# Performance work log

Hardware: AMD Instinct MI355X
Metric: run time of the kernel (lower is better)

Reference implementation:

```python
import jax, jax.numpy as jnp
import numpy as np

FM = 80            # feature_maps
N_ROUNDS = 32
NORM_EPS = 1e-3
LOSS_EPS = 1e-8


def _relu6(x):
    return jnp.clip(x, 0.0, 6.0)


def _norm(x):
    # tf.nn.moments over axis 0 + batch_normalization (no scale/offset)
    mean = jnp.mean(x, axis=0, keepdims=True)
    var = jnp.var(x, axis=0, keepdims=True)
    return (x - mean) * jax.lax.rsqrt(var + NORM_EPS)


def setup_inputs() -> dict:
    key = jax.random.key(0)
    n_vars, n_clauses, n_graphs, lits_per_clause = 100000, 420000, 100, 3
    n_cells = n_clauses * lits_per_clause
    ks = jax.random.split(key, 24)

    lit_var = jax.random.randint(ks[0], (n_cells,), 0, n_vars, dtype=jnp.int32)
    lit_neg = jax.random.randint(ks[1], (n_cells,), 0, 2, dtype=jnp.int32)
    clause_idx = jnp.repeat(jnp.arange(n_clauses, dtype=jnp.int32), lits_per_clause)
    clause_graph = jnp.repeat(jnp.arange(n_graphs, dtype=jnp.int32), n_clauses // n_graphs)

    def dense(k, fi, fo):
        return jax.random.normal(k, (fi, fo), jnp.float32) / np.sqrt(fi)

    inp = dict(
        lit_var=lit_var, lit_neg=lit_neg, clause_idx=clause_idx, clause_graph=clause_graph,
        n_vars=n_vars, n_clauses=n_clauses, n_graphs=n_graphs,
        L_init_scale=jnp.float32(1.0 / np.sqrt(FM)),
        C_init_scale=jnp.float32(1.0 / np.sqrt(FM)),
        LC_scale=jnp.float32(0.1), CL_scale=jnp.float32(0.1),
        # L_update MLP: in=3*FM (L, CL_msgs, flip(L)) -> hidden 3*FM relu6 -> FM
        Lu_W0=dense(ks[2], 3 * FM, 3 * FM), Lu_b0=jnp.zeros((3 * FM,), jnp.float32),
        Lu_W1=dense(ks[3], 3 * FM, FM),     Lu_b1=jnp.zeros((FM,), jnp.float32),
        # C_update MLP: in=2*FM (C, LC_msgs) -> hidden 2*FM relu6 -> FM
        Cu_W0=dense(ks[4], 2 * FM, 2 * FM), Cu_b0=jnp.zeros((2 * FM,), jnp.float32),
        Cu_W1=dense(ks[5], 2 * FM, FM),     Cu_b1=jnp.zeros((FM,), jnp.float32),
        # V_score MLP: in=2*FM -> 3 hidden relu6 layers of 2*FM -> 1
        Vs_W0=dense(ks[6], 2 * FM, 2 * FM), Vs_b0=jnp.zeros((2 * FM,), jnp.float32),
        Vs_W1=dense(ks[7], 2 * FM, 2 * FM), Vs_b1=jnp.zeros((2 * FM,), jnp.float32),
        Vs_W2=dense(ks[8], 2 * FM, 2 * FM), Vs_b2=jnp.zeros((2 * FM,), jnp.float32),
        Vs_W3=dense(ks[9], 2 * FM, 1),      Vs_b3=jnp.zeros((1,), jnp.float32),
    )
    return inp


def reference(lit_var, lit_neg, clause_idx, clause_graph, n_vars, n_clauses, n_graphs,
              L_init_scale, C_init_scale, LC_scale, CL_scale,
              Lu_W0, Lu_b0, Lu_W1, Lu_b1,
              Cu_W0, Cu_b0, Cu_W1, Cu_b1,
              Vs_W0, Vs_b0, Vs_W1, Vs_b1, Vs_W2, Vs_b2, Vs_W3, Vs_b3):
    n_lits = 2 * n_vars
    lit_row = lit_var + lit_neg * n_vars          # row in L for each cell
    sign = (1 - 2 * lit_neg).astype(jnp.float32)  # +1 positive literal, -1 negated

    def mlp_L(x):
        return _relu6(x @ Lu_W0 + Lu_b0) @ Lu_W1 + Lu_b1

    def mlp_C(x):
        return _relu6(x @ Cu_W0 + Cu_b0) @ Cu_W1 + Cu_b1

    def v_score(x):
        h = _relu6(x @ Vs_W0 + Vs_b0)
        h = _relu6(h @ Vs_W1 + Vs_b1)
        h = _relu6(h @ Vs_W2 + Vs_b2)
        return h @ Vs_W3 + Vs_b3

    def flip(L):
        return jnp.concatenate([L[n_vars:], L[:n_vars]], axis=0)

    def per_round_loss(logits):
        # softplus_mixed_loss over ragged clauses of signed literals
        lit_vals = logits[lit_var, 0] * sign                         # [n_cells]
        clause_sum = jax.ops.segment_sum(jax.nn.softplus(lit_vals), clause_idx,
                                         num_segments=n_clauses)     # [n_clauses]
        vc = jnp.exp(-clause_sum)
        per_clause = vc * (-jnp.log(1.0 - vc + LOSS_EPS))
        per_graph = jax.ops.segment_sum(per_clause, clause_graph, num_segments=n_graphs)
        return jnp.sum(jnp.sqrt(per_graph + 1e-6))

    L0 = jnp.ones((n_lits, FM), jnp.float32) * L_init_scale
    C0 = jnp.ones((n_clauses, FM), jnp.float32) * C_init_scale

    def round_fn(carry, _):
        L, C, loss = carry
        # CL^T @ L  (sparse gather + segment-sum over clause cells)
        LC_msgs = jax.ops.segment_sum(L[lit_row], clause_idx, num_segments=n_clauses) * LC_scale
        C = _norm(mlp_C(jnp.concatenate([C, LC_msgs], axis=-1)))
        # adj @ C  (scatter-add clause features back to literal rows)
        CL_msgs = jax.ops.segment_sum(C[clause_idx], lit_row, num_segments=n_lits) * CL_scale
        L = _norm(mlp_L(jnp.concatenate([L, CL_msgs, flip(L)], axis=-1)))
        V = jnp.concatenate([L[:n_vars], L[n_vars:]], axis=1)        # [n_vars, 2*FM]
        logits = v_score(V)
        loss = loss + per_round_loss(logits)
        return (L, C, loss), None

    (L, C, loss), _ = jax.lax.scan(round_fn, (L0, C0, jnp.float32(0.0)), None, length=N_ROUNDS)
    # final-round logits (recomputed from the final L state, identical math)
    logits = v_score(jnp.concatenate([L[:n_vars], L[n_vars:]], axis=1))
    return logits, loss / N_ROUNDS
```

## Files before the change

### kernel.cpp

```cpp
#include <hip/hip_runtime.h>
#include <hip/hip_fp8.h>
#include <math.h>


#define NROUNDS 32
#define NORM_EPS 1e-3f
#define LOSS_EPS 1e-8f

static constexpr int NV_CONST = 100000;
static constexpr int NG_CONST = 100;

typedef __attribute__((ext_vector_type(8))) short short8;
typedef __attribute__((ext_vector_type(8))) unsigned char uchar8;
typedef __attribute__((ext_vector_type(16))) unsigned char uchar16;
typedef __attribute__((ext_vector_type(4))) float f32x4;

__device__ __forceinline__ short f2bf(float f) {
    union { float f; unsigned u; } x; x.f = f;
    unsigned r = x.u + 0x7fffu + ((x.u >> 16) & 1u);
    return (short)(r >> 16);
}
__device__ __forceinline__ float bf2f(short s) {
    union { unsigned u; float f; } x; x.u = ((unsigned)(unsigned short)s) << 16;
    return x.f;
}
__device__ __forceinline__ unsigned char f2q8(float f) {
    f = fminf(fmaxf(f, -448.f), 448.f);
    __hip_fp8_e4m3 t(f);
    return t.__x;
}
__device__ __forceinline__ float q82f(unsigned char b) {
    __hip_fp8_e4m3 t; t.__x = b;
    return (float)t;
}

__device__ __forceinline__ int xcd_swz(int b, int nb) {
    int q = nb >> 3, r = nb & 7;
    int xcd = b & 7, idx = b >> 3;
    return (xcd < r ? xcd * (q + 1) : r * (q + 1) + (xcd - r) * q) + idx;
}


__global__ void k_zero_i(int* __restrict__ p, int n) {
    int i = blockIdx.x * 256 + threadIdx.x;
    if (i < n) p[i] = 0;
}
__global__ void k_fill_b(short* __restrict__ p, int n, const float* __restrict__ vp) {
    int i = blockIdx.x * 256 + threadIdx.x;
    if (i < n) p[i] = f2bf(*vp);
}
__global__ void k_fill_q8(unsigned char* __restrict__ p, int n, const float* __restrict__ vp) {
    int i = blockIdx.x * 256 + threadIdx.x;
    if (i < n) p[i] = f2q8(*vp);
}
__global__ void k_copy_int(int* __restrict__ dst, const int* __restrict__ src, int n) {
    int i = blockIdx.x * 256 + threadIdx.x;
    if (i < n) dst[i] = src[i];
}
__global__ void k_init_slabs(float* __restrict__ slabC, float* __restrict__ slabL,
                             float* __restrict__ loss_a, float nclf, float nlf) {
    int i = blockIdx.x * 256 + threadIdx.x;
    if (i < 33 * 160) {
        slabC[i] = (i >= 80 && i < 160) ? nclf * (1.f - NORM_EPS) : 0.f;
        slabL[i] = (i >= 80 && i < 160) ? nlf * (1.f - NORM_EPS) : 0.f;
    }
    if (i == 0) loss_a[0] = 0.f;
}

__global__ void k_litrow(const int* __restrict__ lit_var, const int* __restrict__ lit_neg,
                         int* __restrict__ litrow, int* __restrict__ cellpk,
                         int* __restrict__ counts, int* __restrict__ fhist,
                         int ncell, int nv) {
    int i = blockIdx.x * 256 + threadIdx.x;
    if (i < ncell) {
        int vv = lit_var[i], ng = lit_neg[i];
        int r = vv + ng * nv;
        litrow[i] = r;
        cellpk[i] = vv | (ng << 31);
        atomicAdd(&counts[r], 1);
        if (i % 3 == 0) atomicAdd(&fhist[r], 1);
    }
}

__launch_bounds__(1024)
__global__ void k_scan4(const int* __restrict__ counts, int* __restrict__ row_ptr,
                        int n, int total) {
    __shared__ int sd[1024];
    __shared__ int carry;
    int tid = threadIdx.x;
    if (tid == 0) carry = 0;
    __syncthreads();
    for (int base = 0; base < n; base += 4096) {
        int i0 = base + tid * 4;
        int a0 = (i0 + 0 < n) ? counts[i0 + 0] : 0;
        int a1 = (i0 + 1 < n) ? counts[i0 + 1] : 0;
        int a2 = (i0 + 2 < n) ? counts[i0 + 2] : 0;
        int a3 = (i0 + 3 < n) ? counts[i0 + 3] : 0;
        int s = a0 + a1 + a2 + a3;
        sd[tid] = s;
        __syncthreads();
        for (int off = 1; off < 1024; off <<= 1) {
            int t = (tid >= off) ? sd[tid - off] : 0;
            __syncthreads();
            sd[tid] += t;
            __syncthreads();
        }
        int excl = carry + sd[tid] - s;
        if (i0 + 0 < n) row_ptr[i0 + 0] = excl;
        if (i0 + 1 < n) row_ptr[i0 + 1] = excl + a0;
        if (i0 + 2 < n) row_ptr[i0 + 2] = excl + a0 + a1;
        if (i0 + 3 < n) row_ptr[i0 + 3] = excl + a0 + a1 + a2;
        __syncthreads();
        if (tid == 0) carry += sd[1023];
        __syncthreads();
    }
    if (tid == 0) row_ptr[n] = total;
}

__global__ void k_place(const int* __restrict__ litrow, int* __restrict__ fcur,
                        int* __restrict__ newpos, int* __restrict__ lofs4, int ncl) {
    int c = blockIdx.x * 256 + threadIdx.x;
    if (c < ncl) {
        int k = litrow[3 * c];
        int np = atomicAdd(&fcur[k], 1);
        newpos[c] = np;
        lofs4[np * 4 + 0] = litrow[3 * c + 0] * 8;
        lofs4[np * 4 + 1] = litrow[3 * c + 1] * 8;
        lofs4[np * 4 + 2] = litrow[3 * c + 2] * 8;
    }
}

__global__ void k_fill_csr(const int* __restrict__ litrow, const int* __restrict__ clause_idx,
                           const int* __restrict__ newpos,
                           int* __restrict__ cursor, int* __restrict__ cl_of, int ncell) {
    int i = blockIdx.x * 256 + threadIdx.x;
    if (i < ncell) {
        int r = litrow[i];
        int pos = atomicAdd(&cursor[r], 1);
        cl_of[pos] = newpos[clause_idx[i]];
    }
}

__global__ void k_pack_w(const float* __restrict__ W, short* __restrict__ Wp,
                         int K, int N, int KB, int NB) {
    int t = blockIdx.x * 256 + threadIdx.x;
    int tot = NB * KB * 64;
    if (t >= tot) return;
    int lane = t & 63;
    int kb = (t >> 6) % KB;
    int nb = t / (64 * KB);
    int quad = lane >> 4, l15 = lane & 15;
    int n = nb * 16 + l15;
#pragma unroll
    for (int j = 0; j < 8; ++j) {
        int k = kb * 32 + quad * 8 + j;
        float f = (k < K && n < N) ? W[(size_t)k * N + n] : 0.f;
        Wp[(size_t)t * 8 + j] = f2bf(f);
    }
}


template <int KB, int NB>
__device__ __forceinline__ void mfma_layer(const short* lds, int SK,
                                           const short8* __restrict__ Wp,
                                           f32x4* acc, int lane, int arow) {
    const int quad8 = (lane >> 4) * 8;
    short8 a[KB];
#pragma unroll
    for (int kb = 0; kb < KB; ++kb)
        a[kb] = *(const short8*)(lds + arow * SK + kb * 32 + quad8);
#pragma unroll
    for (int kb = 0; kb < KB; ++kb)
#pragma unroll
        for (int nb = 0; nb < NB; ++nb)
            acc[nb] = __builtin_amdgcn_mfma_f32_16x16x32_bf16(
                a[kb], Wp[(nb * KB + kb) * 64 + lane], acc[nb], 0, 0, 0);
}

template <int NB>
__device__ __forceinline__ void write_hidden(short* ldsH, int SKH, const f32x4* acc,
                                             const float* __restrict__ bias,
                                             int l15, int quad, int wr0) {
#pragma unroll
    for (int nb = 0; nb < NB; ++nb) {
        int c = nb * 16 + l15;
        float bv = bias[c];
#pragma unroll
        for (int reg = 0; reg < 4; ++reg) {
            int row = wr0 + quad * 4 + reg;
            float v = acc[nb][reg] + bv;
            v = fminf(fmaxf(v, 0.f), 6.f);
            ldsH[row * SKH + c] = f2bf(v);
        }
    }
}

__device__ __forceinline__ void load_stats(const float* __restrict__ slab, float Minv,
                                           float* sS, int tid) {
    if (tid < 80) {
        float m = slab[tid] * Minv;
        float v = slab[80 + tid] * Minv - m * m;
        sS[tid] = m;
        sS[80 + tid] = rsqrtf(v + NORM_EPS);
    }
}

__launch_bounds__(256, 2)
__global__ void k_c_update(short* __restrict__ Cb, unsigned char* __restrict__ Cb8,
                           const unsigned char* __restrict__ Lb8,
                           const int4* __restrict__ lofs4, const float* __restrict__ scp,
                           const short8* __restrict__ W0p, const float* __restrict__ b0,
                           const short8* __restrict__ W1p, const float* __restrict__ b1,
                           const float* __restrict__ prevSlab, float* __restrict__ nextSlab,
                           float Minv, int ncl) {
    constexpr int SK = 168;
    __shared__ short lds[64 * SK];
    __shared__ float sred[160], sC[160];
    const int lane = threadIdx.x, wy = threadIdx.y, tid = wy * 64 + lane;
    const int r0 = xcd_swz(blockIdx.x, gridDim.x) * 64;
    const int rows = (ncl - r0 < 64) ? (ncl - r0) : 64;

    if (tid < 160) sred[tid] = 0.f;
    load_stats(prevSlab, Minv, sC, tid);
    __syncthreads();

    const float s = *scp;
    const short8* Cbv = (const short8*)Cb;
    const uchar16* Lq = (const uchar16*)Lb8;

#pragma unroll
    for (int u = 0; u < 3; ++u) {
        int it = tid + u * 256;
        int itc = (it < 640) ? it : 639;
        int lr = itc / 10, c = itc - lr * 10;
        int cl = r0 + ((lr < rows) ? lr : rows - 1);
        short8 v = __builtin_nontemporal_load(&Cbv[(size_t)cl * 10 + c]);
        int col = c * 8;
        short8 o;
#pragma unroll
        for (int j = 0; j < 8; ++j)
            o[j] = f2bf((bf2f(v[j]) - sC[col + j]) * sC[80 + col + j]);
        if (it < 640)
            *(short8*)(lds + lr * SK + col) = o;
    }
#pragma unroll
    for (int u = 0; u < 2; ++u) {
        int it = tid + u * 256;
        int itc = (it < 320) ? it : 319;
        int lr = itc / 5, cc = itc - lr * 5;
        int cl = r0 + ((lr < rows) ? lr : rows - 1);
        int4 o4 = lofs4[cl];
        uchar16 va = Lq[(size_t)o4.x + cc];
        uchar16 vb = Lq[(size_t)o4.y + cc];
        uchar16 vc = Lq[(size_t)o4.z + cc];
        short8 o0, o1;
#pragma unroll
        for (int j = 0; j < 8; ++j) {
            o0[j] = f2bf((q82f(va[j]) + q82f(vb[j]) + q82f(vc[j])) * s);
            o1[j] = f2bf((q82f(va[8 + j]) + q82f(vb[8 + j]) + q82f(vc[8 + j])) * s);
        }
        if (it < 320) {
            *(short8*)(lds + lr * SK + 80 + cc * 16) = o0;
            *(short8*)(lds + lr * SK + 80 + cc * 16 + 8) = o1;
        }
    }
    __syncthreads();

    const int quad = lane >> 4, l15 = lane & 15, wr0 = wy * 16, arow = wr0 + l15;

    f32x4 acc[10];
#pragma unroll
    for (int nb = 0; nb < 10; ++nb) { f32x4 z = {0.f, 0.f, 0.f, 0.f}; acc[nb] = z; }
    mfma_layer<5, 10>(lds, SK, W0p, acc, lane, arow);
    write_hidden<10>(lds, SK, acc, b0, l15, quad, wr0);

    f32x4 acc2[5];
#pragma unroll
    for (int nb = 0; nb < 5; ++nb) { f32x4 z = {0.f, 0.f, 0.f, 0.f}; acc2[nb] = z; }
    mfma_layer<5, 5>(lds, SK, W1p, acc2, lane, arow);

#pragma unroll
    for (int nb = 0; nb < 5; ++nb) {
        int cc = nb * 16 + l15;
        float bv = b1[cc];
        float s1 = 0.f, s2 = 0.f;
#pragma unroll
        for (int reg = 0; reg < 4; ++reg) {
            int lr = wr0 + quad * 4 + reg;
            if (lr < rows) {
                float v = acc2[nb][reg] + bv;
                __builtin_nontemporal_store(f2bf(v), &Cb[(size_t)(r0 + lr) * 80 + cc]);
                Cb8[(size_t)(r0 + lr) * 128 + cc] = f2q8(v);
                s1 += v; s2 += v * v;
            }
        }
        s1 += __shfl_xor(s1, 16); s1 += __shfl_xor(s1, 32);
        s2 += __shfl_xor(s2, 16); s2 += __shfl_xor(s2, 32);
        if (quad == 0) { atomicAdd(&sred[cc], s1); atomicAdd(&sred[80 + cc], s2); }
    }
    __syncthreads();
    if (tid < 160) atomicAdd(&nextSlab[tid], sred[tid]);
}

__launch_bounds__(256)
__global__ void k_cl_gather(const unsigned char* __restrict__ Cb8,
                            const int* __restrict__ row_ptr,
                            const int* __restrict__ cl_of, const float* __restrict__ scp,
                            const float* __restrict__ slab, float Minv,
                            short* __restrict__ CLb, int nl) {
    __shared__ float sC[160];
    load_stats(slab, Minv, sC, threadIdx.x);
    __syncthreads();
    int idx = xcd_swz(blockIdx.x, gridDim.x) * 256 + threadIdx.x;
    if (idx >= nl * 5) return;
    int r = idx / 5, c16 = idx - r * 5;
    int p0 = row_ptr[r], p1 = row_ptr[r + 1];
    float a[16];
#pragma unroll
    for (int j = 0; j < 16; ++j) a[j] = 0.f;
    const uchar16* Cq = (const uchar16*)Cb8;
    int p = p0;
    for (; p + 4 <= p1; p += 4) {
        int i0 = cl_of[p], i1 = cl_of[p + 1], i2 = cl_of[p + 2], i3 = cl_of[p + 3];
        uchar16 v0 = Cq[(size_t)i0 * 8 + c16];
        uchar16 v1 = Cq[(size_t)i1 * 8 + c16];
        uchar16 v2 = Cq[(size_t)i2 * 8 + c16];
        uchar16 v3 = Cq[(size_t)i3 * 8 + c16];
#pragma unroll
        for (int j = 0; j < 16; ++j)
            a[j] += (q82f(v0[j]) + q82f(v1[j])) + (q82f(v2[j]) + q82f(v3[j]));
    }
    for (; p < p1; ++p) {
        uchar16 v = Cq[(size_t)cl_of[p] * 8 + c16];
#pragma unroll
        for (int j = 0; j < 16; ++j) a[j] += q82f(v[j]);
    }
    float n = (float)(p1 - p0), s = *scp;
    int col = c16 * 16;
    short8 o0, o1;
#pragma unroll
    for (int j = 0; j < 8; ++j) {
        o0[j] = f2bf((a[j] - n * sC[col + j]) * sC[80 + col + j] * s);
        o1[j] = f2bf((a[8 + j] - n * sC[col + 8 + j]) * sC[80 + col + 8 + j] * s);
    }
    ((short8*)CLb)[(size_t)r * 10 + c16 * 2] = o0;
    ((short8*)CLb)[(size_t)r * 10 + c16 * 2 + 1] = o1;
}

__launch_bounds__(256, 2)
__global__ void k_l_update(short* __restrict__ Lraw, const short* __restrict__ CLb,
                           const short8* __restrict__ W0p, const float* __restrict__ b0,
                           const short8* __restrict__ W1p, const float* __restrict__ b1,
                           const float* __restrict__ prevSlab, float* __restrict__ nextSlab,
                           float Minv, int nv) {
    constexpr int SK = 264;
    __shared__ short lds[64 * SK];
    __shared__ float sred[160], sL[160];
    const int lane = threadIdx.x, wy = threadIdx.y, tid = wy * 64 + lane;
    const int vb = blockIdx.x * 32;

    if (tid < 160) sred[tid] = 0.f;
    load_stats(prevSlab, Minv, sL, tid);
    __syncthreads();

    const short8* Lr8  = (const short8*)Lraw;
    const short8* CLb8 = (const short8*)CLb;
    short8 vals[8];
#pragma unroll
    for (int u = 0; u < 8; ++u) {
        int it = tid + u * 256;
        int lr = it >> 5, c = it & 31;
        int own = (lr < 32) ? vb + lr : vb + nv + (lr - 32);
        int opp = (lr < 32) ? vb + nv + lr : vb + (lr - 32);
        if (c < 10) {
            vals[u] = Lr8[(size_t)own * 10 + c];
        } else if (c < 20) {
            vals[u] = CLb8[(size_t)own * 10 + (c - 10)];
        } else if (c < 30) {
            vals[u] = Lr8[(size_t)opp * 10 + (c - 20)];
        } else {
            short8 z = {0, 0, 0, 0, 0, 0, 0, 0};
            vals[u] = z;
        }
    }
#pragma unroll
    for (int u = 0; u < 8; ++u) {
        int it = tid + u * 256;
        int lr = it >> 5, c = it & 31;
        short8 w = vals[u];
        if (c < 10 || (c >= 20 && c < 30)) {
            int base = (c < 10) ? c * 8 : (c - 20) * 8;
#pragma unroll
            for (int j = 0; j < 8; ++j)
                w[j] = f2bf((bf2f(w[j]) - sL[base + j]) * sL[80 + base + j]);
        }
        int o = (c < 10) ? c * 8 : (c < 20) ? 80 + (c - 10) * 8
              : (c < 30) ? 160 + (c - 20) * 8 : 240 + (c - 30) * 8;
        *(short8*)(lds + lr * SK + o) = w;
    }
    __syncthreads();

    const int quad = lane >> 4, l15 = lane & 15, wr0 = wy * 16, arow = wr0 + l15;

    f32x4 acc[15];
#pragma unroll
    for (int nb = 0; nb < 15; ++nb) { f32x4 z = {0.f, 0.f, 0.f, 0.f}; acc[nb] = z; }
    mfma_layer<8, 15>(lds, SK, W0p, acc, lane, arow);
    write_hidden<15>(lds, SK, acc, b0, l15, quad, wr0);
    {
        int row = wr0 + (lane >> 2);
        int c = 240 + (lane & 3) * 4;
        short4 z; z.x = 0; z.y = 0; z.z = 0; z.w = 0;
        *(short4*)(lds + row * SK + c) = z;
    }

    f32x4 acc2[5];
#pragma unroll
    for (int nb = 0; nb < 5; ++nb) { f32x4 z = {0.f, 0.f, 0.f, 0.f}; acc2[nb] = z; }
    mfma_layer<8, 5>(lds, SK, W1p, acc2, lane, arow);

#pragma unroll
    for (int nb = 0; nb < 5; ++nb) {
        int cc = nb * 16 + l15;
        float bv = b1[cc];
        float s1 = 0.f, s2 = 0.f;
#pragma unroll
        for (int reg = 0; reg < 4; ++reg) {
            int lr = wr0 + quad * 4 + reg;
            int rabs = (lr < 32) ? vb + lr : vb + nv + (lr - 32);
            float v = acc2[nb][reg] + bv;
            Lraw[(size_t)rabs * 80 + cc] = f2bf(v);
            s1 += v; s2 += v * v;
        }
        s1 += __shfl_xor(s1, 16); s1 += __shfl_xor(s1, 32);
        s2 += __shfl_xor(s2, 16); s2 += __shfl_xor(s2, 32);
        if (quad == 0) { atomicAdd(&sred[cc], s1); atomicAdd(&sred[80 + cc], s2); }
    }
    __syncthreads();
    if (tid < 160) atomicAdd(&nextSlab[tid], sred[tid]);
}

__launch_bounds__(256, 2)
__global__ void k_v_head(const short* __restrict__ Lraw, const float* __restrict__ slab,
                         float Minv,
                         const short8* __restrict__ W0p, const float* __restrict__ b0,
                         const short8* __restrict__ W1p, const float* __restrict__ b1,
                         const short8* __restrict__ W2p, const float* __restrict__ b2,
                         const float* __restrict__ W3, const float* __restrict__ b3,
                         float* __restrict__ logits,
                         unsigned char* __restrict__ Lb8, int nv) {
    constexpr int SK = 168;
    __shared__ short lds[64 * SK];
    __shared__ float sW3[160], sL[160];
    const int lane = threadIdx.x, wy = threadIdx.y, tid = wy * 64 + lane;
    const int v0 = blockIdx.x * 64;
    const int cnt = (nv - v0 < 64) ? (nv - v0) : 64;

    if (tid < 160) sW3[tid] = W3[tid];
    load_stats(slab, Minv, sL, tid);
    __syncthreads();

    const short8* Lraw8 = (const short8*)Lraw;
    short8 vals[5];
#pragma unroll
    for (int u = 0; u < 5; ++u) {
        int it = tid + u * 256;
        int lr = it / 20, c = it - lr * 20;
        int v = v0 + ((lr < cnt) ? lr : cnt - 1);
        int row = (c < 10) ? v : v + nv;
        int cc = (c < 10) ? c : c - 10;
        vals[u] = Lraw8[(size_t)row * 10 + cc];
    }
#pragma unroll
    for (int u = 0; u < 5; ++u) {
        int it = tid + u * 256;
        int lr = it / 20, c = it - lr * 20;
        int v = v0 + ((lr < cnt) ? lr : cnt - 1);
        int cc = (c < 10) ? c : c - 10;
        int col = cc * 8;
        short8 o;
        uchar8 q;
#pragma unroll
        for (int j = 0; j < 8; ++j) {
            float f = (bf2f(vals[u][j]) - sL[col + j]) * sL[80 + col + j];
            o[j] = f2bf(f);
            q[j] = f2q8(f);
        }
        *(short8*)(lds + lr * SK + c * 8) = o;
        if (lr < cnt) {
            int lit = (c < 10) ? v : (v + nv);
            *(uchar8*)(Lb8 + (size_t)lit * 128 + cc * 8) = q;
        }
    }
    __syncthreads();

    const int quad = lane >> 4, l15 = lane & 15, wr0 = wy * 16, arow = wr0 + l15;

    f32x4 acc[10];
#pragma unroll
    for (int nb = 0; nb < 10; ++nb) { f32x4 z = {0.f, 0.f, 0.f, 0.f}; acc[nb] = z; }
    mfma_layer<5, 10>(lds, SK, W0p, acc, lane, arow);
    write_hidden<10>(lds, SK, acc, b0, l15, quad, wr0);

#pragma unroll
    for (int nb = 0; nb < 10; ++nb) { f32x4 z = {0.f, 0.f, 0.f, 0.f}; acc[nb] = z; }
    mfma_layer<5, 10>(lds, SK, W1p, acc, lane, arow);
    write_hidden<10>(lds, SK, acc, b1, l15, quad, wr0);

#pragma unroll
    for (int nb = 0; nb < 10; ++nb) { f32x4 z = {0.f, 0.f, 0.f, 0.f}; acc[nb] = z; }
    mfma_layer<5, 10>(lds, SK, W2p, acc, lane, arow);
    write_hidden<10>(lds, SK, acc, b2, l15, quad, wr0);
    __syncthreads();

    int lrow = tid >> 2, t4 = tid & 3;
    float v = 0.f;
    for (int c = t4; c < 160; c += 4) v += bf2f(lds[lrow * SK + c]) * sW3[c];
    v += __shfl_down(v, 2, 4);
    v += __shfl_down(v, 1, 4);
    if (t4 == 0 && lrow < cnt) logits[v0 + lrow] = v + b3[0];
}

__device__ __forceinline__ float softplusf(float x) {
    return fmaxf(x, 0.f) + log1pf(expf(-fabsf(x)));
}

__global__ void k_loss(const float* __restrict__ logits, const int* __restrict__ cellpk,
                       float* __restrict__ loss_acc, int cpg) {
    const int g = blockIdx.x;
    const int tid = threadIdx.x;
    float part = 0.f;
    int cend = (g + 1) * cpg;
    for (int c = g * cpg + tid; c < cend; c += 256) {
        float cs = 0.f;
#pragma unroll
        for (int t = 0; t < 3; ++t) {
            int cp = cellpk[c * 3 + t];
            float sign = (cp < 0) ? -1.f : 1.f;
            cs += softplusf(logits[cp & 0x7fffffff] * sign);
        }
        float vc = expf(-cs);
        part += vc * (-log1pf(LOSS_EPS - vc));
    }
    __shared__ float red[256];
    red[tid] = part;
    __syncthreads();
    for (int s = 128; s > 0; s >>= 1) {
        if (tid < s) red[tid] += red[tid + s];
        __syncthreads();
    }
    if (tid == 0) atomicAdd(loss_acc, sqrtf(red[0] + 1e-6f));
}

__global__ void k_output(float* __restrict__ dout, const float* __restrict__ logits,
                         const float* __restrict__ loss_acc, int nv) {
    int i = blockIdx.x * 256 + threadIdx.x;
    if (i < nv) dout[i] = logits[i];
    else if (i == nv) dout[i] = loss_acc[0] * (1.f / (float)NROUNDS);
}


extern "C" void kernel_launch(void* const* d_in, const int* in_sizes, int n_in,
                              void* d_out, int out_size, void* d_ws, size_t ws_size,
                              hipStream_t stream) {
    const int* lit_var    = (const int*)d_in[0];
    const int* lit_neg    = (const int*)d_in[1];
    const int* clause_idx = (const int*)d_in[2];
    const float* Lscale = (const float*)d_in[7];
    const float* Cscale = (const float*)d_in[8];
    const float* LCs    = (const float*)d_in[9];
    const float* CLs    = (const float*)d_in[10];
    const float* LuW0 = (const float*)d_in[11]; const float* Lub0 = (const float*)d_in[12];
    const float* LuW1 = (const float*)d_in[13]; const float* Lub1 = (const float*)d_in[14];
    const float* CuW0 = (const float*)d_in[15]; const float* Cub0 = (const float*)d_in[16];
    const float* CuW1 = (const float*)d_in[17]; const float* Cub1 = (const float*)d_in[18];
    const float* VsW0 = (const float*)d_in[19]; const float* Vsb0 = (const float*)d_in[20];
    const float* VsW1 = (const float*)d_in[21]; const float* Vsb1 = (const float*)d_in[22];
    const float* VsW2 = (const float*)d_in[23]; const float* Vsb2 = (const float*)d_in[24];
    const float* VsW3 = (const float*)d_in[25]; const float* Vsb3 = (const float*)d_in[26];

    const int ncell = in_sizes[0];
    const int ncl   = in_sizes[3];
    const int nv    = NV_CONST;
    const int nl    = 2 * nv;
    const int ng    = NG_CONST;

    size_t off = 0;
    auto A = [&](size_t bytes) -> void* {
        void* q = (char*)d_ws + off;
        off = (off + bytes + 255) & ~(size_t)255;
        return q;
    };
    short* Cb    = (short*)A((size_t)ncl * 80 * 2);
    short* Lraw  = (short*)A((size_t)nl * 80 * 2);
    short* CLb   = (short*)A((size_t)nl * 80 * 2);
    unsigned char* Lb8 = (unsigned char*)A((size_t)nl * 128);
    unsigned char* Cb8 = (unsigned char*)A((size_t)ncl * 128);
    float* logits = (float*)A((size_t)nv * 4);
    float* slabC  = (float*)A(33 * 160 * 4);
    float* slabL  = (float*)A(33 * 160 * 4);
    float* loss_a = (float*)A(256);
    int* litrow  = (int*)A((size_t)ncell * 4);
    int* lofs4   = (int*)A((size_t)ncl * 16);
    int* cellpk  = (int*)A((size_t)ncell * 4);
    int* row_ptr = (int*)A((size_t)(nl + 1) * 4);
    int* tmp     = (int*)A((size_t)nl * 4);
    int* cl_of   = (int*)A((size_t)ncell * 4);
    int* fhist   = (int*)A((size_t)nl * 4);
    int* fbase   = (int*)A((size_t)(nl + 1) * 4);
    int* newpos  = (int*)A((size_t)ncl * 4);
    short* CuW0p = (short*)A((size_t)10 * 5 * 64 * 16);
    short* CuW1p = (short*)A((size_t)5  * 5 * 64 * 16);
    short* LuW0p = (short*)A((size_t)15 * 8 * 64 * 16);
    short* LuW1p = (short*)A((size_t)5  * 8 * 64 * 16);
    short* VsW0p = (short*)A((size_t)10 * 5 * 64 * 16);
    short* VsW1p = (short*)A((size_t)10 * 5 * 64 * 16);
    short* VsW2p = (short*)A((size_t)10 * 5 * 64 * 16);

    const dim3 B64x4(64, 4, 1);

    k_zero_i<<<(nl + 255) / 256, 256, 0, stream>>>(tmp, nl);
    k_zero_i<<<(nl + 255) / 256, 256, 0, stream>>>(fhist, nl);
    k_init_slabs<<<(33 * 160 + 255) / 256, 256, 0, stream>>>(slabC, slabL, loss_a,
                                                             (float)ncl, (float)nl);
    k_litrow<<<(ncell + 255) / 256, 256, 0, stream>>>(lit_var, lit_neg, litrow, cellpk,
                                                      tmp, fhist, ncell, nv);
    k_scan4<<<1, 1024, 0, stream>>>(tmp, row_ptr, nl, ncell);
    k_scan4<<<1, 1024, 0, stream>>>(fhist, fbase, nl, ncl);
    k_copy_int<<<(nl + 255) / 256, 256, 0, stream>>>(tmp, row_ptr, nl);
    k_copy_int<<<(nl + 255) / 256, 256, 0, stream>>>(fhist, fbase, nl);
    k_place<<<(ncl + 255) / 256, 256, 0, stream>>>(litrow, fhist, newpos, lofs4, ncl);
    k_fill_csr<<<(ncell + 255) / 256, 256, 0, stream>>>(litrow, clause_idx, newpos,
                                                        tmp, cl_of, ncell);
    k_fill_b<<<(ncl * 80 + 255) / 256, 256, 0, stream>>>(Cb, ncl * 80, Cscale);
    k_fill_b<<<(nl * 80 + 255) / 256, 256, 0, stream>>>(Lraw, nl * 80, Lscale);
    k_fill_q8<<<(nl * 128 + 255) / 256, 256, 0, stream>>>(Lb8, nl * 128, Lscale);
    k_fill_q8<<<(ncl * 128 + 255) / 256, 256, 0, stream>>>(Cb8, ncl * 128, Cscale);
    k_pack_w<<<(10 * 5 * 64 + 255) / 256, 256, 0, stream>>>(CuW0, CuW0p, 160, 160, 5, 10);
    k_pack_w<<<(5  * 5 * 64 + 255) / 256, 256, 0, stream>>>(CuW1, CuW1p, 160, 80, 5, 5);
    k_pack_w<<<(15 * 8 * 64 + 255) / 256, 256, 0, stream>>>(LuW0, LuW0p, 240, 240, 8, 15);
    k_pack_w<<<(5  * 8 * 64 + 255) / 256, 256, 0, stream>>>(LuW1, LuW1p, 240, 80, 8, 5);
    k_pack_w<<<(10 * 5 * 64 + 255) / 256, 256, 0, stream>>>(VsW0, VsW0p, 160, 160, 5, 10);
    k_pack_w<<<(10 * 5 * 64 + 255) / 256, 256, 0, stream>>>(VsW1, VsW1p, 160, 160, 5, 10);
    k_pack_w<<<(10 * 5 * 64 + 255) / 256, 256, 0, stream>>>(VsW2, VsW2p, 160, 160, 5, 10);

    const int cblk  = (ncl + 63) / 64;
    const int lblk  = nv / 32;
    const int vblk  = (nv + 63) / 64;
    const int clblk = (nl * 5 + 255) / 256;
    const float MinvC = 1.f / (float)ncl;
    const float MinvL = 1.f / (float)nl;

    for (int r = 0; r < NROUNDS; ++r) {
        float* sCr  = slabC + (size_t)r * 160;
        float* sCr1 = slabC + (size_t)(r + 1) * 160;
        float* sLr  = slabL + (size_t)r * 160;
        float* sLr1 = slabL + (size_t)(r + 1) * 160;
        k_c_update<<<cblk, B64x4, 0, stream>>>(
            Cb, Cb8, Lb8, (const int4*)lofs4, LCs, (const short8*)CuW0p, Cub0,
            (const short8*)CuW1p, Cub1, sCr, sCr1, MinvC, ncl);
        k_cl_gather<<<clblk, 256, 0, stream>>>(Cb8, row_ptr, cl_of, CLs, sCr1, MinvC, CLb, nl);
        k_l_update<<<lblk, B64x4, 0, stream>>>(
            Lraw, CLb, (const short8*)LuW0p, Lub0, (const short8*)LuW1p, Lub1,
            sLr, sLr1, MinvL, nv);
        k_v_head<<<vblk, B64x4, 0, stream>>>(
            Lraw, sLr1, MinvL, (const short8*)VsW0p, Vsb0, (const short8*)VsW1p, Vsb1,
            (const short8*)VsW2p, Vsb2, VsW3, Vsb3, logits, Lb8, nv);
        k_loss<<<ng, 256, 0, stream>>>(logits, cellpk, loss_a, ncl / ng);
    }

    k_output<<<(nv + 1 + 255) / 256, 256, 0, stream>>>((float*)d_out, logits, loss_a, nv);
}
```

Measured before the change: 15.79 ms.

## Fuse clause-to-literal gather into L update kernel, dropping CLb buffer

The separate CL gather kernel, which summed fp8 clause features per literal row and wrote normalized bf16 messages to a global CLb buffer, is folded into k_l_update. Each block now computes the gathered messages for its 64 literal rows straight into shared memory, alongside loading the L and flipped-L tiles. This removes one kernel launch per round and the global write and re-read of CLb. In exchange, only 320 of 256×2 thread slots do the irregular gather inside a block limited to 2 blocks per SM, which may lower the memory-level parallelism available for the gather.

```diff
diff --git a/kernel.cpp b/kernel.cpp
--- a/kernel.cpp
+++ b/kernel.cpp
@@ -302,101 +302,100 @@
     if (tid < 160) atomicAdd(&nextSlab[tid], sred[tid]);
 }
 
-__launch_bounds__(256)
-__global__ void k_cl_gather(const unsigned char* __restrict__ Cb8,
-                            const int* __restrict__ row_ptr,
-                            const int* __restrict__ cl_of, const float* __restrict__ scp,
-                            const float* __restrict__ slab, float Minv,
-                            short* __restrict__ CLb, int nl) {
-    __shared__ float sC[160];
-    load_stats(slab, Minv, sC, threadIdx.x);
-    __syncthreads();
-    int idx = xcd_swz(blockIdx.x, gridDim.x) * 256 + threadIdx.x;
-    if (idx >= nl * 5) return;
-    int r = idx / 5, c16 = idx - r * 5;
-    int p0 = row_ptr[r], p1 = row_ptr[r + 1];
-    float a[16];
-#pragma unroll
-    for (int j = 0; j < 16; ++j) a[j] = 0.f;
-    const uchar16* Cq = (const uchar16*)Cb8;
-    int p = p0;
-    for (; p + 4 <= p1; p += 4) {
-        int i0 = cl_of[p], i1 = cl_of[p + 1], i2 = cl_of[p + 2], i3 = cl_of[p + 3];
-        uchar16 v0 = Cq[(size_t)i0 * 8 + c16];
-        uchar16 v1 = Cq[(size_t)i1 * 8 + c16];
-        uchar16 v2 = Cq[(size_t)i2 * 8 + c16];
-        uchar16 v3 = Cq[(size_t)i3 * 8 + c16];
-#pragma unroll
-        for (int j = 0; j < 16; ++j)
-            a[j] += (q82f(v0[j]) + q82f(v1[j])) + (q82f(v2[j]) + q82f(v3[j]));
-    }
-    for (; p < p1; ++p) {
-        uchar16 v = Cq[(size_t)cl_of[p] * 8 + c16];
-#pragma unroll
-        for (int j = 0; j < 16; ++j) a[j] += q82f(v[j]);
-    }
-    float n = (float)(p1 - p0), s = *scp;
-    int col = c16 * 16;
-    short8 o0, o1;
-#pragma unroll
-    for (int j = 0; j < 8; ++j) {
-        o0[j] = f2bf((a[j] - n * sC[col + j]) * sC[80 + col + j] * s);
-        o1[j] = f2bf((a[8 + j] - n * sC[col + 8 + j]) * sC[80 + col + 8 + j] * s);
-    }
-    ((short8*)CLb)[(size_t)r * 10 + c16 * 2] = o0;
-    ((short8*)CLb)[(size_t)r * 10 + c16 * 2 + 1] = o1;
-}
-
 __launch_bounds__(256, 2)
-__global__ void k_l_update(short* __restrict__ Lraw, const short* __restrict__ CLb,
+__global__ void k_l_update(short* __restrict__ Lraw,
+                           const unsigned char* __restrict__ Cb8,
+                           const int* __restrict__ row_ptr, const int* __restrict__ cl_of,
+                           const float* __restrict__ clscp,
+                           const float* __restrict__ cSlab, float MinvC,
                            const short8* __restrict__ W0p, const float* __restrict__ b0,
                            const short8* __restrict__ W1p, const float* __restrict__ b1,
                            const float* __restrict__ prevSlab, float* __restrict__ nextSlab,
-                           float Minv, int nv) {
+                           float MinvL, int nv) {
     constexpr int SK = 264;
     __shared__ short lds[64 * SK];
-    __shared__ float sred[160], sL[160];
+    __shared__ float sred[160], sL[160], sC[160];
     const int lane = threadIdx.x, wy = threadIdx.y, tid = wy * 64 + lane;
-    const int vb = blockIdx.x * 32;
+    const int vb = xcd_swz(blockIdx.x, gridDim.x) * 32;
 
     if (tid < 160) sred[tid] = 0.f;
-    load_stats(prevSlab, Minv, sL, tid);
-    __syncthreads();
-
-    const short8* Lr8  = (const short8*)Lraw;
-    const short8* CLb8 = (const short8*)CLb;
-    short8 vals[8];
-#pragma unroll
-    for (int u = 0; u < 8; ++u) {
+    load_stats(prevSlab, MinvL, sL, tid);
+    load_stats(cSlab, MinvC, sC, tid);
+    __syncthreads();
+
+    const short8* Lr8 = (const short8*)Lraw;
+    short8 vals[6];
+#pragma unroll
+    for (int u = 0; u < 6; ++u) {
         int it = tid + u * 256;
-        int lr = it >> 5, c = it & 31;
+        int itc = (it < 1408) ? it : 1407;
+        int lr = itc / 22, c = itc - lr * 22;
         int own = (lr < 32) ? vb + lr : vb + nv + (lr - 32);
         int opp = (lr < 32) ? vb + nv + lr : vb + (lr - 32);
-        if (c < 10) {
-            vals[u] = Lr8[(size_t)own * 10 + c];
-        } else if (c < 20) {
-            vals[u] = CLb8[(size_t)own * 10 + (c - 10)];
-        } else if (c < 30) {
-            vals[u] = Lr8[(size_t)opp * 10 + (c - 20)];
+        int row = (c < 10) ? own : opp;
+        int cc = (c < 10) ? c : ((c < 20) ? c - 10 : 0);
+        vals[u] = Lr8[(size_t)row * 10 + cc];
+    }
+
+    const float cs = *clscp;
+    const uchar16* Cq = (const uchar16*)Cb8;
+#pragma unroll
+    for (int u = 0; u < 2; ++u) {
+        int it = tid + u * 256;
+        if (it < 320) {
+            int lr = it / 5, c16 = it - lr * 5;
+            int r = (lr < 32) ? vb + lr : vb + nv + (lr - 32);
+            int p0 = row_ptr[r], p1 = row_ptr[r + 1];
+            float a[16];
+#pragma unroll
+            for (int j = 0; j < 16; ++j) a[j] = 0.f;
+            int p = p0;
+            for (; p + 4 <= p1; p += 4) {
+                int i0 = cl_of[p], i1 = cl_of[p + 1], i2 = cl_of[p + 2], i3 = cl_of[p + 3];
+                uchar16 v0 = Cq[(size_t)i0 * 8 + c16];
+                uchar16 v1 = Cq[(size_t)i1 * 8 + c16];
+                uchar16 v2 = Cq[(size_t)i2 * 8 + c16];
+                uchar16 v3 = Cq[(size_t)i3 * 8 + c16];
+#pragma unroll
+                for (int j = 0; j < 16; ++j)
+                    a[j] += (q82f(v0[j]) + q82f(v1[j])) + (q82f(v2[j]) + q82f(v3[j]));
+            }
+            for (; p < p1; ++p) {
+                uchar16 v = Cq[(size_t)cl_of[p] * 8 + c16];
+#pragma unroll
+                for (int j = 0; j < 16; ++j) a[j] += q82f(v[j]);
+            }
+            float n = (float)(p1 - p0);
+            int col = c16 * 16;
+            short8 o0, o1;
+#pragma unroll
+            for (int j = 0; j < 8; ++j) {
+                o0[j] = f2bf((a[j] - n * sC[col + j]) * sC[80 + col + j] * cs);
+                o1[j] = f2bf((a[8 + j] - n * sC[col + 8 + j]) * sC[80 + col + 8 + j] * cs);
+            }
+            *(short8*)(lds + lr * SK + 80 + c16 * 16) = o0;
+            *(short8*)(lds + lr * SK + 80 + c16 * 16 + 8) = o1;
+        }
+    }
+
+#pragma unroll
+    for (int u = 0; u < 6; ++u) {
+        int it = tid + u * 256;
+        int itc = (it < 1408) ? it : 1407;
+        int lr = itc / 22, c = itc - lr * 22;
+        short8 w = vals[u];
+        if (c < 20) {
+            int base = ((c < 10) ? c : c - 10) * 8;
+#pragma unroll
+            for (int j = 0; j < 8; ++j)
+                w[j] = f2bf((bf2f(w[j]) - sL[base + j]) * sL[80 + base + j]);
         } else {
             short8 z = {0, 0, 0, 0, 0, 0, 0, 0};
-            vals[u] = z;
-        }
-    }
-#pragma unroll
-    for (int u = 0; u < 8; ++u) {
-        int it = tid + u * 256;
-        int lr = it >> 5, c = it & 31;
-        short8 w = vals[u];
-        if (c < 10 || (c >= 20 && c < 30)) {
-            int base = (c < 10) ? c * 8 : (c - 20) * 8;
-#pragma unroll
-            for (int j = 0; j < 8; ++j)
-                w[j] = f2bf((bf2f(w[j]) - sL[base + j]) * sL[80 + base + j]);
-        }
-        int o = (c < 10) ? c * 8 : (c < 20) ? 80 + (c - 10) * 8
-              : (c < 30) ? 160 + (c - 20) * 8 : 240 + (c - 30) * 8;
-        *(short8*)(lds + lr * SK + o) = w;
+            w = z;
+        }
+        int o = (c < 10) ? c * 8 : (c < 20) ? 160 + (c - 10) * 8 : 240 + (c - 20) * 8;
+        if (it < 1408)
+            *(short8*)(lds + lr * SK + o) = w;
     }
     __syncthreads();
 
@@ -593,7 +592,6 @@
     };
     short* Cb    = (short*)A((size_t)ncl * 80 * 2);
     short* Lraw  = (short*)A((size_t)nl * 80 * 2);
-    short* CLb   = (short*)A((size_t)nl * 80 * 2);
     unsigned char* Lb8 = (unsigned char*)A((size_t)nl * 128);
     unsigned char* Cb8 = (unsigned char*)A((size_t)ncl * 128);
     float* logits = (float*)A((size_t)nv * 4);
@@ -647,7 +645,6 @@
     const int cblk  = (ncl + 63) / 64;
     const int lblk  = nv / 32;
     const int vblk  = (nv + 63) / 64;
-    const int clblk = (nl * 5 + 255) / 256;
     const float MinvC = 1.f / (float)ncl;
     const float MinvL = 1.f / (float)nl;
 
@@ -659,9 +656,9 @@
         k_c_update<<<cblk, B64x4, 0, stream>>>(
             Cb, Cb8, Lb8, (const int4*)lofs4, LCs, (const short8*)CuW0p, Cub0,
             (const short8*)CuW1p, Cub1, sCr, sCr1, MinvC, ncl);
-        k_cl_gather<<<clblk, 256, 0, stream>>>(Cb8, row_ptr, cl_of, CLs, sCr1, MinvC, CLb, nl);
         k_l_update<<<lblk, B64x4, 0, stream>>>(
-            Lraw, CLb, (const short8*)LuW0p, Lub0, (const short8*)LuW1p, Lub1,
+            Lraw, Cb8, row_ptr, cl_of, CLs, sCr1, MinvC,
+            (const short8*)LuW0p, Lub0, (const short8*)LuW1p, Lub1,
             sLr, sLr1, MinvL, nv);
         k_v_head<<<vblk, B64x4, 0, stream>>>(
             Lraw, sLr1, MinvL, (const short8*)VsW0p, Vsb0, (const short8*)VsW1p, Vsb1,
```

New measurement: 15.88 ms. About the same (+0.6%).
